# Performance work log

Measured on AMD Instinct MI355X. Metric: run time of the kernel, lower is better.

Reference implementation:

```python
import jax, jax.numpy as jnp
import numpy as np

N, K, D = 32768, 1024, 256
TAU = 1.0          # gumbel-softmax temperature (torch default)
KL_WEIGHT = 1.0    # settings.kl_weight stand-in
EPS = 1e-6


def setup_inputs() -> dict:
    key = jax.random.key(0)
    k1, k2, k3 = jax.random.split(key, 3)
    latents = jax.random.normal(k1, (N, D), dtype=jnp.float32)
    # torch init: uniform_(-1/num_protos, 1/num_protos)
    prototypes = jax.random.uniform(k2, (K, D), dtype=jnp.float32,
                                    minval=-1.0 / K, maxval=1.0 / K)
    u = jax.random.uniform(k3, (N, K), dtype=jnp.float32,
                           minval=1e-10, maxval=1.0)
    gumbel = -jnp.log(-jnp.log(u))  # Gumbel(0,1) noise
    return {"latents": latents, "prototypes": prototypes, "gumbel": gumbel}


def reference(latents, prototypes, gumbel):
    # squared euclidean distances latents[:,None,:] - prototypes -> [N, K]
    # expanded form (same math, avoids [N,K,D] intermediate):
    d2 = (jnp.sum(latents * latents, axis=-1, keepdims=True)
          - 2.0 * latents @ prototypes.T
          + jnp.sum(prototypes * prototypes, axis=-1))
    logits = (-d2 + gumbel) / TAU
    logprobs = jax.nn.log_softmax(logits, axis=-1)      # [N, K]
    y_soft = jnp.exp(logprobs)
    # hard=True straight-through one-hot
    idx = jnp.argmax(y_soft, axis=-1)
    y_hard = jax.nn.one_hot(idx, K, dtype=y_soft.dtype)
    onehot = y_hard - jax.lax.stop_gradient(y_soft) + y_soft
    quantized = onehot @ prototypes                     # [N, D]

    # prior over codes (batch mean of probs), broadcast to all rows
    prior = jnp.mean(y_soft + EPS, axis=0)              # [K]
    # KLDivLoss(reduction='batchmean')(logprobs, prior):
    # mean over rows of sum_k prior_k * (log prior_k - logprobs_k)
    capacity = jnp.mean(jnp.sum(prior * (jnp.log(prior) - logprobs), axis=-1))
    ent = -jnp.sum(prior * jnp.log(prior))
    # settings.epoch <= 5000 branch: subtract entropy term
    vq_loss = KL_WEIGHT * capacity - 0.001 * ent
    return quantized, vq_loss
```

## Files before the change

### kernel.cpp

```cpp
#include <hip/hip_runtime.h>
#include <hip/hip_bf16.h>
#include <stdint.h>

#define NN 32768
#define KK 1024
#define DD 256
#define BM 32
#define CHUNK 64
#define NCHUNK (KK / CHUNK)
#define NTHR 512
#define NRB (NN / BM)

#define LXS 0
#define LPS 16384
#define LA_TOT 49152
#define SC_MAXP 0
#define SC_ZP   1024
#define SC_MI   1536

#define BMF 16
#define LSS 8192
#define LRM (LSS + 32768)
#define LRI (LRM + 64)
#define FLPS 41216
#define LTOT_PRE  41216
#define LTOT_NPRE (41216 + 65536)

#define PB_OFF   12288
#define SBUF_OFF 536576
#define LZ_OFF   (SBUF_OFF + (size_t)NRB * NCHUNK * 512 * 8)
#define WS_FULL  (LZ_OFF + (size_t)NN * 4)
#define WS_PRE   (PB_OFF + (size_t)KK * DD * 2)

typedef __attribute__((ext_vector_type(8))) short bf16x8;
typedef __attribute__((ext_vector_type(4))) float f32x4;

__device__ __forceinline__ uint32_t pkbf2(float a, float b) {
    uint32_t ua = __builtin_bit_cast(uint32_t, a);
    uint32_t ub = __builtin_bit_cast(uint32_t, b);
    ua = (ua + 0x7fffu + ((ua >> 16) & 1u)) >> 16;
    ub = (ub + 0x7fffu + ((ub >> 16) & 1u)) >> 16;
    return ua | (ub << 16);
}
__device__ __forceinline__ float ubf(uint32_t h) {
    return __builtin_bit_cast(float, h << 16);
}

__global__ void vq_init(const float* __restrict__ protos, float* __restrict__ ws) {
    int k = blockIdx.x * 256 + threadIdx.x;
    const float4* p4 = reinterpret_cast<const float4*>(protos + (size_t)k * DD);
    float s = 0.f;
#pragma unroll 8
    for (int j = 0; j < DD / 4; ++j) {
        float4 v = p4[j];
        s = fmaf(v.x, v.x, s); s = fmaf(v.y, v.y, s);
        s = fmaf(v.z, v.z, s); s = fmaf(v.w, v.w, s);
    }
    ws[k] = s;
    ws[KK + k] = 0.f;
    ws[2 * KK + k] = 0.f;
}

__global__ void vq_cvt(const float* __restrict__ protos, uint32_t* __restrict__ pb) {
    int idx = blockIdx.x * 256 + threadIdx.x;
    const float4* s = reinterpret_cast<const float4*>(protos + (size_t)idx * 8);
    float4 a = s[0], b = s[1];
    uint4 v;
    v.x = pkbf2(a.x, a.y); v.y = pkbf2(a.z, a.w);
    v.z = pkbf2(b.x, b.y); v.w = pkbf2(b.z, b.w);
    reinterpret_cast<uint4*>(pb)[idx] = v;
}

__global__ __launch_bounds__(NTHR) void vq_mainA(const float* __restrict__ latents,
                                                 const float* __restrict__ protos,
                                                 const float* __restrict__ gumbel,
                                                 float* __restrict__ ws,
                                                 float* __restrict__ out) {
    __shared__ __align__(16) unsigned char sm[LA_TOT];
    const int t = threadIdx.x;
    const int lane = t & 63;
    const int w = t >> 6;
    const int rb = blockIdx.x;
    const int n0 = rb * BM;
    const int l15 = lane & 15;
    const int l4 = lane >> 4;
    const int wq = w & 3;
    const int wh = w >> 2;
    const int xr = wh * 16 + l15;
    const float* np2 = ws;
    const uint4* pb = reinterpret_cast<const uint4*>((char*)ws + PB_OFF);
    uint2* Sb = reinterpret_cast<uint2*>((char*)ws + SBUF_OFF);
    float* lzb = reinterpret_cast<float*>((char*)ws + LZ_OFF);

    {
        int row = t >> 4;
        int g0 = (t & 15) * 2;
#pragma unroll
        for (int j = 0; j < 2; ++j) {
            int g = g0 + j;
            const float4* src = reinterpret_cast<const float4*>(
                latents + (size_t)(n0 + row) * DD + g * 8);
            float4 a = src[0], b = src[1];
            uint4 v; v.x = pkbf2(a.x, a.y); v.y = pkbf2(a.z, a.w);
            v.z = pkbf2(b.x, b.y); v.w = pkbf2(b.z, b.w);
            *reinterpret_cast<uint4*>(sm + LXS + row * 512 + ((g ^ (row & 7)) << 4)) = v;
        }
    }

    const int pr = wq * 16 + l15;
    float z = 0.f, m = -3.4e38f; int mi = 0;

    for (int c = 0; c < NCHUNK; ++c) {
        __syncthreads();
#pragma unroll
        for (int i = 0; i < 4; ++i) {
            int G = t + NTHR * i;
            int p = G >> 5, g = G & 31;
            *reinterpret_cast<uint4*>(sm + LPS + p * 512 + ((g ^ (p & 7)) << 4)) =
                pb[(size_t)(c * CHUNK + p) * 32 + g];
        }
        __syncthreads();

        const int pg0 = c * CHUNK + wq * 16 + l4 * 4;
        float4 q4 = *reinterpret_cast<const float4*>(np2 + pg0);
        float4 g4 = *reinterpret_cast<const float4*>(gumbel + (size_t)(n0 + xr) * KK + pg0);

        f32x4 acc = {0.f, 0.f, 0.f, 0.f};
#pragma unroll
        for (int ks = 0; ks < 8; ++ks) {
            int gi = ks * 4 + l4;
            bf16x8 af = *reinterpret_cast<bf16x8*>(sm + LPS + pr * 512 + ((gi ^ (pr & 7)) << 4));
            bf16x8 b0 = *reinterpret_cast<bf16x8*>(sm + LXS + xr * 512 + ((gi ^ (xr & 7)) << 4));
            acc = __builtin_amdgcn_mfma_f32_16x16x32_bf16(af, b0, acc, 0, 0, 0);
        }
        float s0 = fmaf(2.f, acc.x, -q4.x) + g4.x;
        float s1 = fmaf(2.f, acc.y, -q4.y) + g4.y;
        float s2 = fmaf(2.f, acc.z, -q4.z) + g4.z;
        float s3 = fmaf(2.f, acc.w, -q4.w) + g4.w;
        z += __expf(s0) + __expf(s1) + __expf(s2) + __expf(s3);
        if (s0 > m) { m = s0; mi = pg0; }
        if (s1 > m) { m = s1; mi = pg0 + 1; }
        if (s2 > m) { m = s2; mi = pg0 + 2; }
        if (s3 > m) { m = s3; mi = pg0 + 3; }
        uint2 pk; pk.x = pkbf2(s0, s1); pk.y = pkbf2(s2, s3);
        Sb[((size_t)rb * NCHUNK + c) * 512 + t] = pk;
    }
    __syncthreads();

#pragma unroll
    for (int off = 16; off <= 32; off <<= 1) {
        float om = __shfl_xor(m, off); int oi = __shfl_xor(mi, off);
        if (om > m || (om == m && oi < mi)) { m = om; mi = oi; }
        z += __shfl_xor(z, off);
    }
    if (lane < 16) {
        *reinterpret_cast<float*>(sm + SC_MAXP + (xr * 4 + wq) * 8) = m;
        *reinterpret_cast<int*>(sm + SC_MAXP + (xr * 4 + wq) * 8 + 4) = mi;
        *reinterpret_cast<float*>(sm + SC_ZP + (xr * 4 + wq) * 4) = z;
    }
    __syncthreads();
    if (t < 32) {
        float mm = -3.4e38f; int mmi = 0; float Z = 0.f;
#pragma unroll
        for (int j = 0; j < 4; ++j) {
            float om = *reinterpret_cast<float*>(sm + SC_MAXP + (t * 4 + j) * 8);
            int oi = *reinterpret_cast<int*>(sm + SC_MAXP + (t * 4 + j) * 8 + 4);
            if (om > mm || (om == mm && oi < mmi)) { mm = om; mmi = oi; }
            Z += *reinterpret_cast<float*>(sm + SC_ZP + (t * 4 + j) * 4);
        }
        lzb[n0 + t] = __logf(Z);
        *reinterpret_cast<int*>(sm + SC_MI + t * 4) = mmi;
    }
    __syncthreads();

    {
        int row = t >> 4, v = t & 15;
        int idx = *reinterpret_cast<int*>(sm + SC_MI + row * 4);
        const float4* src = reinterpret_cast<const float4*>(protos + (size_t)idx * DD + v * 16);
        float4* dst = reinterpret_cast<float4*>(out + (size_t)(n0 + row) * DD + v * 16);
#pragma unroll
        for (int j = 0; j < 4; ++j) dst[j] = src[j];
    }
}

__global__ __launch_bounds__(NTHR) void vq_colsum(float* __restrict__ ws) {
    const int t = threadIdx.x;
    const int l15 = t & 15;
    const int c = blockIdx.x & 15;
    const int rg = blockIdx.x >> 4;
    const uint2* Sb = reinterpret_cast<const uint2*>((char*)ws + SBUF_OFF);
    const float* lzb = reinterpret_cast<const float*>((char*)ws + LZ_OFF);
    float* colsum_y = ws + KK;
    float* colsum_lp = ws + 2 * KK;
    const int xr = ((t >> 8) & 1) * 16 + l15;

    float sy0 = 0.f, sy1 = 0.f, sy2 = 0.f, sy3 = 0.f;
    float sl0 = 0.f, sl1 = 0.f, sl2 = 0.f, sl3 = 0.f;
    for (int i = 0; i < NRB / 32; ++i) {
        int rb = rg * (NRB / 32) + i;
        uint2 v = Sb[((size_t)rb * NCHUNK + c) * 512 + t];
        float lz = lzb[rb * BM + xr];
        float a0 = ubf(v.x & 0xffffu) - lz, a1 = ubf(v.x >> 16) - lz;
        float a2 = ubf(v.y & 0xffffu) - lz, a3 = ubf(v.y >> 16) - lz;
        sy0 += __expf(a0); sy1 += __expf(a1); sy2 += __expf(a2); sy3 += __expf(a3);
        sl0 += a0; sl1 += a1; sl2 += a2; sl3 += a3;
    }
#pragma unroll
    for (int off = 1; off < 16; off <<= 1) {
        sy0 += __shfl_xor(sy0, off); sy1 += __shfl_xor(sy1, off);
        sy2 += __shfl_xor(sy2, off); sy3 += __shfl_xor(sy3, off);
        sl0 += __shfl_xor(sl0, off); sl1 += __shfl_xor(sl1, off);
        sl2 += __shfl_xor(sl2, off); sl3 += __shfl_xor(sl3, off);
    }
    if (l15 == 0) {
        int cb = c * CHUNK + ((t >> 6) & 3) * 16 + ((t >> 4) & 3) * 4;
        atomicAdd(&colsum_y[cb],     sy0); atomicAdd(&colsum_y[cb + 1], sy1);
        atomicAdd(&colsum_y[cb + 2], sy2); atomicAdd(&colsum_y[cb + 3], sy3);
        atomicAdd(&colsum_lp[cb],     sl0); atomicAdd(&colsum_lp[cb + 1], sl1);
        atomicAdd(&colsum_lp[cb + 2], sl2); atomicAdd(&colsum_lp[cb + 3], sl3);
    }
}

template<bool PRE>
__global__ __launch_bounds__(NTHR) void vq_mainT(const float* __restrict__ latents,
                                                 const float* __restrict__ protos,
                                                 const float* __restrict__ gumbel,
                                                 float* __restrict__ ws,
                                                 float* __restrict__ out) {
    __shared__ __align__(16) unsigned char sm[PRE ? LTOT_PRE : LTOT_NPRE];
    const int t = threadIdx.x;
    const int lane = t & 63;
    const int w = t >> 6;
    const int n0 = blockIdx.x * BMF;
    const int l15 = lane & 15;
    const int l4 = lane >> 4;
    const float* np2 = ws;
    float* colsum_y = ws + KK;
    float* colsum_lp = ws + 2 * KK;
    const uint4* pb = reinterpret_cast<const uint4*>((char*)ws + PB_OFF);

    {
        int row = t >> 5, g = t & 31;
        const float4* src = reinterpret_cast<const float4*>(
            latents + (size_t)(n0 + row) * DD + g * 8);
        float4 a = src[0], b = src[1];
        uint4 v; v.x = pkbf2(a.x, a.y); v.y = pkbf2(a.z, a.w);
        v.z = pkbf2(b.x, b.y); v.w = pkbf2(b.z, b.w);
        *reinterpret_cast<uint4*>(sm + row * 512 + ((g ^ (row & 7)) << 4)) = v;
    }
    __syncthreads();

    const int pr = w * 16 + l15;
    const int cwbase = w * 16 + l4 * 4;

    for (int c = 0; c < 8; ++c) {
        if (!PRE) {
            __syncthreads();
#pragma unroll
            for (int i = 0; i < 8; ++i) {
                int G = t + NTHR * i;
                int p = G >> 5, g = G & 31;
                const float4* src = reinterpret_cast<const float4*>(
                    protos + (size_t)(c * 128 + p) * DD + g * 8);
                float4 a = src[0], b = src[1];
                uint4 v; v.x = pkbf2(a.x, a.y); v.y = pkbf2(a.z, a.w);
                v.z = pkbf2(b.x, b.y); v.w = pkbf2(b.z, b.w);
                *reinterpret_cast<uint4*>(sm + FLPS + p * 512 + ((g ^ (p & 7)) << 4)) = v;
            }
            __syncthreads();
        }
        const int pg0 = c * 128 + cwbase;
        float4 q4 = *reinterpret_cast<const float4*>(np2 + pg0);
        float4 g4 = *reinterpret_cast<const float4*>(gumbel + (size_t)(n0 + l15) * KK + pg0);

        f32x4 acc = {0.f, 0.f, 0.f, 0.f};
        if (PRE) {
            const uint4* afp = pb + (size_t)(c * 128 + pr) * 32;
#pragma unroll
            for (int ks = 0; ks < 8; ++ks) {
                int gi = ks * 4 + l4;
                bf16x8 af = __builtin_bit_cast(bf16x8, afp[gi]);
                bf16x8 b0 = *reinterpret_cast<bf16x8*>(
                    sm + l15 * 512 + ((gi ^ (l15 & 7)) << 4));
                acc = __builtin_amdgcn_mfma_f32_16x16x32_bf16(af, b0, acc, 0, 0, 0);
            }
        } else {
#pragma unroll
            for (int ks = 0; ks < 8; ++ks) {
                int gi = ks * 4 + l4;
                bf16x8 af = *reinterpret_cast<bf16x8*>(
                    sm + FLPS + pr * 512 + ((gi ^ (pr & 7)) << 4));
                bf16x8 b0 = *reinterpret_cast<bf16x8*>(
                    sm + l15 * 512 + ((gi ^ (l15 & 7)) << 4));
                acc = __builtin_amdgcn_mfma_f32_16x16x32_bf16(af, b0, acc, 0, 0, 0);
            }
        }
        {
            const int Gs = pg0 >> 2;
            uint2 pk;
            pk.x = pkbf2(fmaf(2.f, acc.x, -q4.x) + g4.x, fmaf(2.f, acc.y, -q4.y) + g4.y);
            pk.y = pkbf2(fmaf(2.f, acc.z, -q4.z) + g4.z, fmaf(2.f, acc.w, -q4.w) + g4.w);
            *reinterpret_cast<uint2*>(sm + LSS + l15 * 2048 + ((Gs ^ ((l15 & 7) << 1)) << 3)) = pk;
        }
    }
    __syncthreads();

    {
        int row = t >> 5, v = t & 31;
        int sw = (row & 7) << 1;
        uint2 d[8];
#pragma unroll
        for (int j = 0; j < 8; ++j) {
            int G = v + 32 * j;
            d[j] = *reinterpret_cast<uint2*>(sm + LSS + row * 2048 + ((G ^ sw) << 3));
        }
        float m = -3.4e38f; int mi = 0;
#pragma unroll
        for (int j = 0; j < 8; ++j) {
            int c0 = (v + 32 * j) * 4;
            float f0 = ubf(d[j].x & 0xffffu), f1 = ubf(d[j].x >> 16);
            float f2 = ubf(d[j].y & 0xffffu), f3 = ubf(d[j].y >> 16);
            if (f0 > m) { m = f0; mi = c0; }
            if (f1 > m) { m = f1; mi = c0 + 1; }
            if (f2 > m) { m = f2; mi = c0 + 2; }
            if (f3 > m) { m = f3; mi = c0 + 3; }
        }
#pragma unroll
        for (int off = 1; off < 32; off <<= 1) {
            float om = __shfl_xor(m, off);
            int oi = __shfl_xor(mi, off);
            if (om > m || (om == m && oi < mi)) { m = om; mi = oi; }
        }
        float se = 0.f;
#pragma unroll
        for (int j = 0; j < 8; ++j) {
            se += __expf(ubf(d[j].x & 0xffffu) - m);
            se += __expf(ubf(d[j].x >> 16) - m);
            se += __expf(ubf(d[j].y & 0xffffu) - m);
            se += __expf(ubf(d[j].y >> 16) - m);
        }
#pragma unroll
        for (int off = 1; off < 32; off <<= 1) se += __shfl_xor(se, off);
        if (v == 0) {
            *reinterpret_cast<float*>(sm + LRM + row * 4) = m + __logf(se);
            *reinterpret_cast<int*>(sm + LRI + row * 4) = mi;
        }
    }
    __syncthreads();

#pragma unroll
    for (int h = 0; h < 2; ++h) {
        int col = t + h * NTHR;
        int G = col >> 2;
        int e2 = (col & 3) << 1;
        float sy = 0.f, slp = 0.f;
#pragma unroll 8
        for (int r = 0; r < BMF; ++r) {
            uint32_t hv = *reinterpret_cast<uint16_t*>(
                sm + LSS + r * 2048 + ((G ^ ((r & 7) << 1)) << 3) + e2);
            float lz = *reinterpret_cast<float*>(sm + LRM + r * 4);
            float lp = ubf(hv) - lz;
            slp += lp;
            sy += __expf(lp);
        }
        atomicAdd(&colsum_y[col], sy);
        atomicAdd(&colsum_lp[col], slp);
    }

    {
        int row = t >> 5, v = t & 31;
        int idx = *reinterpret_cast<int*>(sm + LRI + row * 4);
        const float4* src = reinterpret_cast<const float4*>(protos + (size_t)idx * DD + v * 8);
        float4* dst = reinterpret_cast<float4*>(out + (size_t)(n0 + row) * DD + v * 8);
        dst[0] = src[0];
        dst[1] = src[1];
    }
}

__global__ void vq_final(const float* __restrict__ ws,
                         float* __restrict__ out, int out_size) {
    __shared__ float part[4];
    int t = threadIdx.x;
    const float invN = 1.0f / (float)NN;
    float a = 0.f;
    for (int j = 0; j < 4; ++j) {
        int k = t + j * 256;
        float prior = fmaf(ws[KK + k], invN, 1e-6f);
        float Lk = ws[2 * KK + k] * invN;
        a += prior * (1.001f * __logf(prior) - Lk);
    }
#pragma unroll
    for (int off = 32; off >= 1; off >>= 1) a += __shfl_xor(a, off);
    if ((t & 63) == 0) part[t >> 6] = a;
    __syncthreads();
    if (t == 0) {
        out[out_size - 1] = part[0] + part[1] + part[2] + part[3];
    }
}

extern "C" void kernel_launch(void* const* d_in, const int* in_sizes, int n_in,
                              void* d_out, int out_size, void* d_ws, size_t ws_size,
                              hipStream_t stream) {
    (void)in_sizes; (void)n_in;
    const float* latents = (const float*)d_in[0];
    const float* protos  = (const float*)d_in[1];
    const float* gumbel  = (const float*)d_in[2];
    float* out           = (float*)d_out;
    float* ws            = (float*)d_ws;

    vq_init<<<dim3(4), dim3(256), 0, stream>>>(protos, ws);
    if (ws_size >= WS_FULL) {
        vq_cvt<<<dim3(KK * DD / 2048), dim3(256), 0, stream>>>(
            protos, (uint32_t*)((char*)d_ws + PB_OFF));
        vq_mainA<<<dim3(NRB), dim3(NTHR), 0, stream>>>(
            latents, protos, gumbel, ws, out);
        vq_colsum<<<dim3(NCHUNK * 32), dim3(NTHR), 0, stream>>>(ws);
    } else if (ws_size >= WS_PRE) {
        vq_cvt<<<dim3(KK * DD / 2048), dim3(256), 0, stream>>>(
            protos, (uint32_t*)((char*)d_ws + PB_OFF));
        vq_mainT<true><<<dim3(NN / BMF), dim3(NTHR), 0, stream>>>(
            latents, protos, gumbel, ws, out);
    } else {
        vq_mainT<false><<<dim3(NN / BMF), dim3(NTHR), 0, stream>>>(
            latents, protos, gumbel, ws, out);
    }
    vq_final<<<dim3(1), dim3(256), 0, stream>>>(ws, out, out_size);
}
```

Measured before the change: 134.1 us.

## Hold latent fragments in registers and double prototype chunk per block in vq_mainA

```diff
diff --git a/kernel.cpp b/kernel.cpp
--- a/kernel.cpp
+++ b/kernel.cpp
@@ -6,19 +6,18 @@
 #define KK 1024
 #define DD 256
 #define BM 32
-#define CHUNK 64
+#define CHUNK 128
 #define NCHUNK (KK / CHUNK)
 #define NTHR 512
 #define NRB (NN / BM)
 
+#define A_MAXP 65536
+#define A_ZP   67584
+#define A_MI   68608
+#define LA_TOT 68736
+
+#define BMF 16
 #define LXS 0
-#define LPS 16384
-#define LA_TOT 49152
-#define SC_MAXP 0
-#define SC_ZP   1024
-#define SC_MI   1536
-
-#define BMF 16
 #define LSS 8192
 #define LRM (LSS + 32768)
 #define LRI (LRM + 64)
@@ -28,7 +27,8 @@
 
 #define PB_OFF   12288
 #define SBUF_OFF 536576
-#define LZ_OFF   (SBUF_OFF + (size_t)NRB * NCHUNK * 512 * 8)
+#define SBUF_BYTES ((size_t)NRB * NCHUNK * 2 * 512 * 8)
+#define LZ_OFF   (SBUF_OFF + SBUF_BYTES)
 #define WS_FULL  (LZ_OFF + (size_t)NN * 4)
 #define WS_PRE   (PB_OFF + (size_t)KK * DD * 2)
 
@@ -84,9 +84,6 @@
     const int n0 = rb * BM;
     const int l15 = lane & 15;
     const int l4 = lane >> 4;
-    const int wq = w & 3;
-    const int wh = w >> 2;
-    const int xr = wh * 16 + l15;
     const float* np2 = ws;
     const uint4* pb = reinterpret_cast<const uint4*>((char*)ws + PB_OFF);
     uint2* Sb = reinterpret_cast<uint2*>((char*)ws + SBUF_OFF);
@@ -103,79 +100,107 @@
             float4 a = src[0], b = src[1];
             uint4 v; v.x = pkbf2(a.x, a.y); v.y = pkbf2(a.z, a.w);
             v.z = pkbf2(b.x, b.y); v.w = pkbf2(b.z, b.w);
-            *reinterpret_cast<uint4*>(sm + LXS + row * 512 + ((g ^ (row & 7)) << 4)) = v;
-        }
-    }
-
-    const int pr = wq * 16 + l15;
-    float z = 0.f, m = -3.4e38f; int mi = 0;
+            *reinterpret_cast<uint4*>(sm + row * 512 + ((g ^ (row & 7)) << 4)) = v;
+        }
+    }
+    __syncthreads();
+    const int xsw = l15 & 7;
+#define LDX(r, k) (*reinterpret_cast<bf16x8*>(sm + (r) * 512 + ((((k) * 4 + l4) ^ xsw) << 4)))
+    bf16x8 xa0 = LDX(l15, 0), xa1 = LDX(l15, 1), xa2 = LDX(l15, 2), xa3 = LDX(l15, 3);
+    bf16x8 xa4 = LDX(l15, 4), xa5 = LDX(l15, 5), xa6 = LDX(l15, 6), xa7 = LDX(l15, 7);
+    bf16x8 xb0 = LDX(16 + l15, 0), xb1 = LDX(16 + l15, 1), xb2 = LDX(16 + l15, 2), xb3 = LDX(16 + l15, 3);
+    bf16x8 xb4 = LDX(16 + l15, 4), xb5 = LDX(16 + l15, 5), xb6 = LDX(16 + l15, 6), xb7 = LDX(16 + l15, 7);
+#undef LDX
+
+    const int pr = w * 16 + l15;
+    const int cwbase = w * 16 + l4 * 4;
+    float z0 = 0.f, m0 = -3.4e38f; int mi0 = 0;
+    float z1 = 0.f, m1 = -3.4e38f; int mi1 = 0;
 
     for (int c = 0; c < NCHUNK; ++c) {
         __syncthreads();
 #pragma unroll
-        for (int i = 0; i < 4; ++i) {
+        for (int i = 0; i < 8; ++i) {
             int G = t + NTHR * i;
             int p = G >> 5, g = G & 31;
-            *reinterpret_cast<uint4*>(sm + LPS + p * 512 + ((g ^ (p & 7)) << 4)) =
+            *reinterpret_cast<uint4*>(sm + p * 512 + ((g ^ (p & 7)) << 4)) =
                 pb[(size_t)(c * CHUNK + p) * 32 + g];
         }
+        const int pg0 = c * CHUNK + cwbase;
+        float4 q4 = *reinterpret_cast<const float4*>(np2 + pg0);
+        float4 g40 = *reinterpret_cast<const float4*>(gumbel + (size_t)(n0 + l15) * KK + pg0);
+        float4 g41 = *reinterpret_cast<const float4*>(gumbel + (size_t)(n0 + 16 + l15) * KK + pg0);
         __syncthreads();
 
-        const int pg0 = c * CHUNK + wq * 16 + l4 * 4;
-        float4 q4 = *reinterpret_cast<const float4*>(np2 + pg0);
-        float4 g4 = *reinterpret_cast<const float4*>(gumbel + (size_t)(n0 + xr) * KK + pg0);
-
-        f32x4 acc = {0.f, 0.f, 0.f, 0.f};
-#pragma unroll
-        for (int ks = 0; ks < 8; ++ks) {
-            int gi = ks * 4 + l4;
-            bf16x8 af = *reinterpret_cast<bf16x8*>(sm + LPS + pr * 512 + ((gi ^ (pr & 7)) << 4));
-            bf16x8 b0 = *reinterpret_cast<bf16x8*>(sm + LXS + xr * 512 + ((gi ^ (xr & 7)) << 4));
-            acc = __builtin_amdgcn_mfma_f32_16x16x32_bf16(af, b0, acc, 0, 0, 0);
-        }
-        float s0 = fmaf(2.f, acc.x, -q4.x) + g4.x;
-        float s1 = fmaf(2.f, acc.y, -q4.y) + g4.y;
-        float s2 = fmaf(2.f, acc.z, -q4.z) + g4.z;
-        float s3 = fmaf(2.f, acc.w, -q4.w) + g4.w;
-        z += __expf(s0) + __expf(s1) + __expf(s2) + __expf(s3);
-        if (s0 > m) { m = s0; mi = pg0; }
-        if (s1 > m) { m = s1; mi = pg0 + 1; }
-        if (s2 > m) { m = s2; mi = pg0 + 2; }
-        if (s3 > m) { m = s3; mi = pg0 + 3; }
-        uint2 pk; pk.x = pkbf2(s0, s1); pk.y = pkbf2(s2, s3);
-        Sb[((size_t)rb * NCHUNK + c) * 512 + t] = pk;
-    }
-    __syncthreads();
+        f32x4 acc0 = {0.f, 0.f, 0.f, 0.f}, acc1 = {0.f, 0.f, 0.f, 0.f};
+#define KSTEP(k, xa, xb) { \
+        bf16x8 af = *reinterpret_cast<bf16x8*>(sm + pr * 512 + ((((k) * 4 + l4) ^ (pr & 7)) << 4)); \
+        acc0 = __builtin_amdgcn_mfma_f32_16x16x32_bf16(af, xa, acc0, 0, 0, 0); \
+        acc1 = __builtin_amdgcn_mfma_f32_16x16x32_bf16(af, xb, acc1, 0, 0, 0); }
+        KSTEP(0, xa0, xb0) KSTEP(1, xa1, xb1) KSTEP(2, xa2, xb2) KSTEP(3, xa3, xb3)
+        KSTEP(4, xa4, xb4) KSTEP(5, xa5, xb5) KSTEP(6, xa6, xb6) KSTEP(7, xa7, xb7)
+#undef KSTEP
+
+        float s0 = fmaf(2.f, acc0.x, -q4.x) + g40.x;
+        float s1 = fmaf(2.f, acc0.y, -q4.y) + g40.y;
+        float s2 = fmaf(2.f, acc0.z, -q4.z) + g40.z;
+        float s3 = fmaf(2.f, acc0.w, -q4.w) + g40.w;
+        z0 += __expf(s0) + __expf(s1) + __expf(s2) + __expf(s3);
+        if (s0 > m0) { m0 = s0; mi0 = pg0; }
+        if (s1 > m0) { m0 = s1; mi0 = pg0 + 1; }
+        if (s2 > m0) { m0 = s2; mi0 = pg0 + 2; }
+        if (s3 > m0) { m0 = s3; mi0 = pg0 + 3; }
+        uint2 pk0; pk0.x = pkbf2(s0, s1); pk0.y = pkbf2(s2, s3);
+        Sb[(((size_t)rb * NCHUNK + c) * 2 + 0) * 512 + t] = pk0;
+        float u0 = fmaf(2.f, acc1.x, -q4.x) + g41.x;
+        float u1 = fmaf(2.f, acc1.y, -q4.y) + g41.y;
+        float u2 = fmaf(2.f, acc1.z, -q4.z) + g41.z;
+        float u3 = fmaf(2.f, acc1.w, -q4.w) + g41.w;
+        z1 += __expf(u0) + __expf(u1) + __expf(u2) + __expf(u3);
+        if (u0 > m1) { m1 = u0; mi1 = pg0; }
+        if (u1 > m1) { m1 = u1; mi1 = pg0 + 1; }
+        if (u2 > m1) { m1 = u2; mi1 = pg0 + 2; }
+        if (u3 > m1) { m1 = u3; mi1 = pg0 + 3; }
+        uint2 pk1; pk1.x = pkbf2(u0, u1); pk1.y = pkbf2(u2, u3);
+        Sb[(((size_t)rb * NCHUNK + c) * 2 + 1) * 512 + t] = pk1;
+    }
 
 #pragma unroll
     for (int off = 16; off <= 32; off <<= 1) {
-        float om = __shfl_xor(m, off); int oi = __shfl_xor(mi, off);
-        if (om > m || (om == m && oi < mi)) { m = om; mi = oi; }
-        z += __shfl_xor(z, off);
-    }
+        float om = __shfl_xor(m0, off); int oi = __shfl_xor(mi0, off);
+        if (om > m0 || (om == m0 && oi < mi0)) { m0 = om; mi0 = oi; }
+        om = __shfl_xor(m1, off); oi = __shfl_xor(mi1, off);
+        if (om > m1 || (om == m1 && oi < mi1)) { m1 = om; mi1 = oi; }
+        z0 += __shfl_xor(z0, off);
+        z1 += __shfl_xor(z1, off);
+    }
+    __syncthreads();
     if (lane < 16) {
-        *reinterpret_cast<float*>(sm + SC_MAXP + (xr * 4 + wq) * 8) = m;
-        *reinterpret_cast<int*>(sm + SC_MAXP + (xr * 4 + wq) * 8 + 4) = mi;
-        *reinterpret_cast<float*>(sm + SC_ZP + (xr * 4 + wq) * 4) = z;
+        *reinterpret_cast<float*>(sm + A_MAXP + (l15 * 8 + w) * 8) = m0;
+        *reinterpret_cast<int*>(sm + A_MAXP + (l15 * 8 + w) * 8 + 4) = mi0;
+        *reinterpret_cast<float*>(sm + A_MAXP + ((16 + l15) * 8 + w) * 8) = m1;
+        *reinterpret_cast<int*>(sm + A_MAXP + ((16 + l15) * 8 + w) * 8 + 4) = mi1;
+        *reinterpret_cast<float*>(sm + A_ZP + (l15 * 8 + w) * 4) = z0;
+        *reinterpret_cast<float*>(sm + A_ZP + ((16 + l15) * 8 + w) * 4) = z1;
     }
     __syncthreads();
     if (t < 32) {
         float mm = -3.4e38f; int mmi = 0; float Z = 0.f;
 #pragma unroll
-        for (int j = 0; j < 4; ++j) {
-            float om = *reinterpret_cast<float*>(sm + SC_MAXP + (t * 4 + j) * 8);
-            int oi = *reinterpret_cast<int*>(sm + SC_MAXP + (t * 4 + j) * 8 + 4);
+        for (int j = 0; j < 8; ++j) {
+            float om = *reinterpret_cast<float*>(sm + A_MAXP + (t * 8 + j) * 8);
+            int oi = *reinterpret_cast<int*>(sm + A_MAXP + (t * 8 + j) * 8 + 4);
             if (om > mm || (om == mm && oi < mmi)) { mm = om; mmi = oi; }
-            Z += *reinterpret_cast<float*>(sm + SC_ZP + (t * 4 + j) * 4);
+            Z += *reinterpret_cast<float*>(sm + A_ZP + (t * 8 + j) * 4);
         }
         lzb[n0 + t] = __logf(Z);
-        *reinterpret_cast<int*>(sm + SC_MI + t * 4) = mmi;
+        *reinterpret_cast<int*>(sm + A_MI + t * 4) = mmi;
     }
     __syncthreads();
 
     {
         int row = t >> 4, v = t & 15;
-        int idx = *reinterpret_cast<int*>(sm + SC_MI + row * 4);
+        int idx = *reinterpret_cast<int*>(sm + A_MI + row * 4);
         const float4* src = reinterpret_cast<const float4*>(protos + (size_t)idx * DD + v * 16);
         float4* dst = reinterpret_cast<float4*>(out + (size_t)(n0 + row) * DD + v * 16);
 #pragma unroll
@@ -186,24 +211,26 @@
 __global__ __launch_bounds__(NTHR) void vq_colsum(float* __restrict__ ws) {
     const int t = threadIdx.x;
     const int l15 = t & 15;
-    const int c = blockIdx.x & 15;
-    const int rg = blockIdx.x >> 4;
+    const int c = blockIdx.x & 7;
+    const int rg = blockIdx.x >> 3;
     const uint2* Sb = reinterpret_cast<const uint2*>((char*)ws + SBUF_OFF);
     const float* lzb = reinterpret_cast<const float*>((char*)ws + LZ_OFF);
     float* colsum_y = ws + KK;
     float* colsum_lp = ws + 2 * KK;
-    const int xr = ((t >> 8) & 1) * 16 + l15;
 
     float sy0 = 0.f, sy1 = 0.f, sy2 = 0.f, sy3 = 0.f;
     float sl0 = 0.f, sl1 = 0.f, sl2 = 0.f, sl3 = 0.f;
     for (int i = 0; i < NRB / 32; ++i) {
         int rb = rg * (NRB / 32) + i;
-        uint2 v = Sb[((size_t)rb * NCHUNK + c) * 512 + t];
-        float lz = lzb[rb * BM + xr];
-        float a0 = ubf(v.x & 0xffffu) - lz, a1 = ubf(v.x >> 16) - lz;
-        float a2 = ubf(v.y & 0xffffu) - lz, a3 = ubf(v.y >> 16) - lz;
-        sy0 += __expf(a0); sy1 += __expf(a1); sy2 += __expf(a2); sy3 += __expf(a3);
-        sl0 += a0; sl1 += a1; sl2 += a2; sl3 += a3;
+#pragma unroll
+        for (int h = 0; h < 2; ++h) {
+            uint2 v = Sb[(((size_t)rb * NCHUNK + c) * 2 + h) * 512 + t];
+            float lz = lzb[rb * BM + h * 16 + l15];
+            float a0 = ubf(v.x & 0xffffu) - lz, a1 = ubf(v.x >> 16) - lz;
+            float a2 = ubf(v.y & 0xffffu) - lz, a3 = ubf(v.y >> 16) - lz;
+            sy0 += __expf(a0); sy1 += __expf(a1); sy2 += __expf(a2); sy3 += __expf(a3);
+            sl0 += a0; sl1 += a1; sl2 += a2; sl3 += a3;
+        }
     }
 #pragma unroll
     for (int off = 1; off < 16; off <<= 1) {
@@ -213,7 +240,8 @@
         sl2 += __shfl_xor(sl2, off); sl3 += __shfl_xor(sl3, off);
     }
     if (l15 == 0) {
-        int cb = c * CHUNK + ((t >> 6) & 3) * 16 + ((t >> 4) & 3) * 4;
+        int w = t >> 6, l4 = (t & 63) >> 4;
+        int cb = c * CHUNK + w * 16 + l4 * 4;
         atomicAdd(&colsum_y[cb],     sy0); atomicAdd(&colsum_y[cb + 1], sy1);
         atomicAdd(&colsum_y[cb + 2], sy2); atomicAdd(&colsum_y[cb + 3], sy3);
         atomicAdd(&colsum_lp[cb],     sl0); atomicAdd(&colsum_lp[cb + 1], sl1);
@@ -246,7 +274,7 @@
         float4 a = src[0], b = src[1];
         uint4 v; v.x = pkbf2(a.x, a.y); v.y = pkbf2(a.z, a.w);
         v.z = pkbf2(b.x, b.y); v.w = pkbf2(b.z, b.w);
-        *reinterpret_cast<uint4*>(sm + row * 512 + ((g ^ (row & 7)) << 4)) = v;
+        *reinterpret_cast<uint4*>(sm + LXS + row * 512 + ((g ^ (row & 7)) << 4)) = v;
     }
     __syncthreads();
 
@@ -281,7 +309,7 @@
                 int gi = ks * 4 + l4;
                 bf16x8 af = __builtin_bit_cast(bf16x8, afp[gi]);
                 bf16x8 b0 = *reinterpret_cast<bf16x8*>(
-                    sm + l15 * 512 + ((gi ^ (l15 & 7)) << 4));
+                    sm + LXS + l15 * 512 + ((gi ^ (l15 & 7)) << 4));
                 acc = __builtin_amdgcn_mfma_f32_16x16x32_bf16(af, b0, acc, 0, 0, 0);
             }
         } else {
@@ -291,7 +319,7 @@
                 bf16x8 af = *reinterpret_cast<bf16x8*>(
                     sm + FLPS + pr * 512 + ((gi ^ (pr & 7)) << 4));
                 bf16x8 b0 = *reinterpret_cast<bf16x8*>(
-                    sm + l15 * 512 + ((gi ^ (l15 & 7)) << 4));
+                    sm + LXS + l15 * 512 + ((gi ^ (l15 & 7)) << 4));
                 acc = __builtin_amdgcn_mfma_f32_16x16x32_bf16(af, b0, acc, 0, 0, 0);
             }
         }
```

Measured after the change: 124.8 us. 1.07x faster.
